# Optimization experiments

Hardware: AMD Instinct MI355X
Metric: run time of the kernel (lower is better)

## Reference

```python
import jax, jax.numpy as jnp
from jax import lax
import numpy as np

B, C, H, W = 8, 32, 512, 256
HEAD = 64
NUM_PEAKS, RADIUS, THRESH = 18, 5, 0.1
BN_EPS = 1e-5


def setup_inputs() -> dict:
    key = jax.random.key(0)
    ks = jax.random.split(key, 8)
    f32 = jnp.float32
    return {
        "x": jax.random.normal(ks[0], (B, C, H, W), f32),
        # fc_hm head params
        "w1_hm": jax.random.normal(ks[1], (HEAD, C, 3, 3), f32) * 0.05,
        "b1_hm": jnp.zeros((HEAD,), f32),
        "g_hm": jnp.ones((HEAD,), f32),
        "be_hm": jnp.zeros((HEAD,), f32),
        "m_hm": jnp.zeros((HEAD,), f32),
        "v_hm": jnp.ones((HEAD,), f32),
        "w2_hm": jax.random.normal(ks[2], (2, HEAD, 1, 1), f32) * 0.05,
        "b2_hm": jnp.zeros((2,), f32),
        # fc_vec head params
        "w1_vec": jax.random.normal(ks[3], (HEAD, C, 3, 3), f32) * 0.05,
        "b1_vec": jnp.zeros((HEAD,), f32),
        "g_vec": jnp.ones((HEAD,), f32),
        "be_vec": jnp.zeros((HEAD,), f32),
        "m_vec": jnp.zeros((HEAD,), f32),
        "v_vec": jnp.ones((HEAD,), f32),
        "w2_vec": jax.random.normal(ks[4], (2, HEAD, 1, 1), f32) * 0.05,
        "b2_vec": jnp.zeros((2,), f32),
    }


def _conv(x, w, b):
    y = lax.conv_general_dilated(x, w, (1, 1), 'SAME',
                                 dimension_numbers=('NCHW', 'OIHW', 'NCHW'))
    return y + b[None, :, None, None]


def _head(x, w1, b1, g, be, m, v, w2, b2):
    # conv3x3 -> BN(eval) -> ReLU -> (dropout=identity) -> conv final_kernel
    h = _conv(x, w1, b1)
    h = g[None, :, None, None] * (h - m[None, :, None, None]) \
        * lax.rsqrt(v + BN_EPS)[None, :, None, None] + be[None, :, None, None]
    h = jax.nn.relu(h)
    return _conv(h, w2, b2)


def _extract_peaks(hm):
    # hm: [H, W] -> peaks [NUM_PEAKS, 2] as (x, y); iterative argmax + square suppression
    ys = jnp.arange(H)[:, None]
    xs = jnp.arange(W)[None, :]

    def step(hmw, _):
        flat = hmw.reshape(-1)
        idx = jnp.argmax(flat)
        mval = flat[idx]
        y = idx // W
        x = idx % W
        valid = mval > THRESH
        peak = jnp.where(valid,
                         jnp.stack([x, y]).astype(hmw.dtype),
                         jnp.zeros((2,), hmw.dtype))
        sup = (jnp.abs(ys - y) <= RADIUS) & (jnp.abs(xs - x) <= RADIUS)
        hmw = jnp.where(valid & sup, jnp.zeros((), hmw.dtype), hmw)
        return hmw, peak

    _, peaks = lax.scan(step, hm, None, length=NUM_PEAKS)
    return peaks


def _order_points(points):
    # points: [N, 2]; pack valid points sorted by y descending, zeros at the end
    valid = points.sum(axis=1) != 0
    key_y = jnp.where(valid, points[:, 1], -jnp.inf)
    order = jnp.argsort(-key_y)
    p = points[order]
    return jnp.where(valid[order][:, None], p, jnp.zeros((), p.dtype))


def reference(x, w1_hm, b1_hm, g_hm, be_hm, m_hm, v_hm, w2_hm, b2_hm,
              w1_vec, b1_vec, g_vec, be_vec, m_vec, v_vec, w2_vec, b2_vec):
    dual_hm = jax.nn.sigmoid(_head(x, w1_hm, b1_hm, g_hm, be_hm, m_hm, v_hm, w2_hm, b2_hm))  # [B,2,H,W]
    vec_ind = _head(x, w1_vec, b1_vec, g_vec, be_vec, m_vec, v_vec, w2_vec, b2_vec)          # [B,2,H,W]

    peaks = jax.vmap(_extract_peaks)(dual_hm.reshape(B * 2, H, W)).reshape(B, 2, NUM_PEAKS, 2)
    upper = jax.vmap(_order_points)(peaks[:, 0])  # [B,18,2]
    lower = jax.vmap(_order_points)(peaks[:, 1])  # [B,18,2]
    mid = (upper + lower) / 2
    return dual_hm, upper, lower, mid, vec_ind
```

## Files before the change

### kernel.cpp

```cpp
#include <hip/hip_runtime.h>

typedef _Float16 f16;
typedef _Float16 f16x8 __attribute__((ext_vector_type(8)));
typedef float f32x4 __attribute__((ext_vector_type(4)));

#define Bn 8
#define Him 512
#define Wim 256
#define NPK 18
#define RAD 5
#define PTHRESH 0.1f
#define BN_EPS 1e-5f

#define SZ_HM   (Bn*2*Him*Wim)
#define OFF_UP  (SZ_HM)
#define OFF_LO  (OFF_UP + Bn*NPK*2)
#define OFF_MID (OFF_LO + Bn*NPK*2)
#define OFF_VEC (OFF_MID + Bn*NPK*2)

#define PH (Him + 2)
#define PW (Wim + 2)
#define XH_ELT ((size_t)Bn * PH * PW * 32)
#define XH_BYTES (XH_ELT * 2)
#define WBYTES 73728
#define WS_NEED (XH_BYTES + WBYTES + 4096)

#define WS_WBYTES 73728
#define XCOLS 258
#define XSTR  40

template <int CTRL>
__device__ __forceinline__ void red2_dpp(float& v, int& r) {
    int ov  = __builtin_amdgcn_update_dpp(0, __float_as_int(v), CTRL, 0xF, 0xF, true);
    int orr = __builtin_amdgcn_update_dpp(0, r, CTRL, 0xF, 0xF, true);
    float fv = __int_as_float(ov);
    if (fv > v || (fv == v && orr < r)) { v = fv; r = orr; }
}
__device__ __forceinline__ void red2_shfl(float& v, int& r, const int off) {
    float fv = __shfl_xor(v, off);
    int  orr = __shfl_xor(r, off);
    if (fv > v || (fv == v && orr < r)) { v = fv; r = orr; }
}
__device__ __forceinline__ void argred64(float& v, int& r) {
    red2_dpp<0xB1>(v, r);
    red2_dpp<0x4E>(v, r);
    red2_dpp<0x141>(v, r);
    red2_dpp<0x140>(v, r);
    red2_shfl(v, r, 16);
    red2_shfl(v, r, 32);
}


__global__ __launch_bounds__(256) void xform_kernel(
    const float* __restrict__ x, f16* __restrict__ xh)
{
    int e = blockIdx.x * 256 + threadIdx.x;
    if (e >= Bn * PH * PW * 4) return;
    int cb  = e & 3;
    int pxl = e >> 2;
    int b   = pxl / (PH * PW);
    int rem = pxl - b * (PH * PW);
    int yy  = rem / PW;
    int xx  = rem - yy * PW;
    int yv = yy - 1, xv = xx - 1;
    f16x8 hv;
    if ((unsigned)yv < (unsigned)Him && (unsigned)xv < (unsigned)Wim) {
        const float* sp = x + (((size_t)b * 32 + cb * 8) * Him + yv) * Wim + xv;
#pragma unroll
        for (int j = 0; j < 8; ++j) hv[j] = (f16)sp[(size_t)j * Him * Wim];
    } else {
#pragma unroll
        for (int j = 0; j < 8; ++j) hv[j] = (f16)0.f;
    }
    *(f16x8*)&xh[(size_t)pxl * 32 + cb * 8] = hv;
}

__global__ __launch_bounds__(256) void prep4_kernel(
    const float* __restrict__ w1_hm, const float* __restrict__ b1_hm,
    const float* __restrict__ g_hm,  const float* __restrict__ be_hm,
    const float* __restrict__ m_hm,  const float* __restrict__ v_hm,
    const float* __restrict__ w1_vec, const float* __restrict__ b1_vec,
    const float* __restrict__ g_vec,  const float* __restrict__ be_vec,
    const float* __restrict__ m_vec,  const float* __restrict__ v_vec,
    const float* __restrict__ w2_hm,  const float* __restrict__ w2_vec,
    void* __restrict__ wreg)
{
    f16* wf = (f16*)wreg;
    float* btf = (float*)((char*)wreg + WBYTES);
    float* waf = btf + 128;
    float* wbf = btf + 256;

    int e = blockIdx.x * 256 + threadIdx.x;
    int rs = e >> 12;
    int rem = e & 4095;
    int n = rem >> 5;
    int c = rem & 31;

    float g, vv, v;
    if (n < 64) { g = g_hm[n]; vv = v_hm[n]; v = w1_hm[(n * 32 + c) * 9 + rs]; }
    else { int j = n - 64; g = g_vec[j]; vv = v_vec[j]; v = w1_vec[(j * 32 + c) * 9 + rs]; }
    float al = g * rsqrtf(vv + BN_EPS);
    int byte = rs * 8192 + n * 64 + c * 2;
    byte ^= (n & 7) << 4;
    wf[byte >> 1] = (f16)(v * al);

    if (e < 128) {
        int nn = e;
        float gg, be, m, vvv, b1;
        if (nn < 64) { gg = g_hm[nn]; be = be_hm[nn]; m = m_hm[nn]; vvv = v_hm[nn]; b1 = b1_hm[nn]; }
        else { int j = nn - 64; gg = g_vec[j]; be = be_vec[j]; m = m_vec[j]; vvv = v_vec[j]; b1 = b1_vec[j]; }
        float a = gg * rsqrtf(vvv + BN_EPS);
        btf[nn] = a * (b1 - m) + be;
        if (nn < 64) { waf[nn] = w2_hm[nn]; wbf[nn] = w2_hm[64 + nn]; }
        else { int j = nn - 64; waf[nn] = w2_vec[j]; wbf[nn] = w2_vec[64 + j]; }
    }
}

__global__ __launch_bounds__(512, 2) void conv7_kernel(
    const f16* __restrict__ xh, const f16* __restrict__ wsw,
    const float* __restrict__ btf, const float* __restrict__ waf,
    const float* __restrict__ wbf,
    const float* __restrict__ b2_hm, const float* __restrict__ b2_vec,
    float* __restrict__ out)
{
    __shared__ __align__(16) f16 s_w[9 * 128 * 32];
    __shared__ __align__(16) f16 s_in[10 * 130 * 32];

    const int hw = blockIdx.x;
    const int logical = (hw & 7) * 128 + (hw >> 3);
    const int b    = logical >> 7;
    const int idx  = logical & 127;
    const int strip = idx >> 1;
    const int half  = idx & 1;
    const int y0  = strip * 8;
    const int x0h = half * 128;

    const int tid  = threadIdx.x;
    const int lane = tid & 63;
    const int wv   = tid >> 6;

    {
        const float4* src = (const float4*)wsw;
        float4* dst = (float4*)s_w;
#pragma unroll
        for (int i = 0; i < 9; ++i) dst[tid + 512 * i] = src[tid + 512 * i];
    }
    {
        const char* xb = (const char*)(xh + (size_t)b * PH * (PW * 32));
        char* sb = (char*)s_in;
        for (int i = tid; i < 5200; i += 512) {
            int row = i / 520;
            int r2  = i - row * 520;
            int px  = r2 >> 2;
            int bo  = (r2 & 3) << 4;
            f16x8 v = *(const f16x8*)(xb + (((size_t)(y0 + row) * PW + (x0h + px)) << 6) + bo);
            int la = ((row * 130 + px) << 6) + bo;
            la ^= (px & 7) << 4;
            *(f16x8*)(sb + la) = v;
        }
    }
    __syncthreads();

    const int l15 = lane & 15;
    const int g   = lane >> 4;
    const int khB = g << 4;
    const int sxz = ((l15 << 6) + khB) ^ ((l15 & 7) << 4);
    const char* swb = (const char*)s_w;
    const char* sib = (const char*)s_in;

    float* outhm  = out + ((size_t)b * 2) * Him * Wim + (y0 + wv) * Wim + x0h;
    float* outvec = out + OFF_VEC + ((size_t)b * 2) * Him * Wim + (y0 + wv) * Wim + x0h;

#pragma unroll 1
    for (int xseg = 0; xseg < 2; ++xseg) {
        const int px0s = xseg << 6;

        f32x4 acc[8][4];
#pragma unroll
        for (int ct = 0; ct < 8; ++ct)
#pragma unroll
            for (int nt = 0; nt < 4; ++nt) acc[ct][nt] = (f32x4){0.f, 0.f, 0.f, 0.f};

#pragma unroll 1
        for (int rr = 0; rr < 3; ++rr) {
#pragma unroll 1
            for (int ss = 0; ss < 3; ++ss) {
                f16x8 af[4];
#pragma unroll
                for (int nt = 0; nt < 4; ++nt) {
                    int pxl = px0s + nt * 16 + l15 + ss;
                    int la = (((wv + rr) * 130 + pxl) << 6) + khB;
                    la ^= (pxl & 7) << 4;
                    af[nt] = *(const f16x8*)(sib + la);
                }
                const char* wtap = swb + (rr * 3 + ss) * 8192 + sxz;
#pragma unroll
                for (int ct = 0; ct < 8; ++ct) {
                    f16x8 wfr = *(const f16x8*)(wtap + ct * 1024);
                    acc[ct][0] = __builtin_amdgcn_mfma_f32_16x16x32_f16(wfr, af[0], acc[ct][0], 0, 0, 0);
                    acc[ct][1] = __builtin_amdgcn_mfma_f32_16x16x32_f16(wfr, af[1], acc[ct][1], 0, 0, 0);
                    acc[ct][2] = __builtin_amdgcn_mfma_f32_16x16x32_f16(wfr, af[2], acc[ct][2], 0, 0, 0);
                    acc[ct][3] = __builtin_amdgcn_mfma_f32_16x16x32_f16(wfr, af[3], acc[ct][3], 0, 0, 0);
                }
            }
        }

        float s[4][4];
#pragma unroll
        for (int nt = 0; nt < 4; ++nt)
#pragma unroll
            for (int o = 0; o < 4; ++o) s[nt][o] = 0.f;

        const int cb0 = g << 2;
#pragma unroll
        for (int ct = 0; ct < 8; ++ct) {
            const float4 bt4 = *(const float4*)&btf[ct * 16 + cb0];
            const float4 wa4 = *(const float4*)&waf[ct * 16 + cb0];
            const float4 wb4 = *(const float4*)&wbf[ct * 16 + cb0];
            float btq[4] = { bt4.x, bt4.y, bt4.z, bt4.w };
            float waq[4] = { wa4.x, wa4.y, wa4.z, wa4.w };
            float wbq[4] = { wb4.x, wb4.y, wb4.z, wb4.w };
#pragma unroll
            for (int nt = 0; nt < 4; ++nt) {
#pragma unroll
                for (int q = 0; q < 4; ++q) {
                    float h = fmaxf(acc[ct][nt][q] + btq[q], 0.f);
                    if (ct < 4) {
                        s[nt][0] = fmaf(waq[q], h, s[nt][0]);
                        s[nt][1] = fmaf(wbq[q], h, s[nt][1]);
                    } else {
                        s[nt][2] = fmaf(waq[q], h, s[nt][2]);
                        s[nt][3] = fmaf(wbq[q], h, s[nt][3]);
                    }
                }
            }
        }
#pragma unroll
        for (int nt = 0; nt < 4; ++nt)
#pragma unroll
            for (int o = 0; o < 4; ++o) {
                s[nt][o] += __shfl_xor(s[nt][o], 16);
                s[nt][o] += __shfl_xor(s[nt][o], 32);
            }

        const float bh0 = b2_hm[0], bh1 = b2_hm[1], bv0 = b2_vec[0], bv1 = b2_vec[1];
        if (g == 0) {
#pragma unroll
            for (int nt = 0; nt < 4; ++nt) {
                int px = px0s + nt * 16 + l15;
                float e = __expf(-(s[nt][0] + bh0));
                outhm[px] = 1.f / (1.f + e);
            }
        } else if (g == 1) {
#pragma unroll
            for (int nt = 0; nt < 4; ++nt) {
                int px = px0s + nt * 16 + l15;
                float e = __expf(-(s[nt][1] + bh1));
                outhm[Him * Wim + px] = 1.f / (1.f + e);
            }
        } else if (g == 2) {
#pragma unroll
            for (int nt = 0; nt < 4; ++nt) {
                int px = px0s + nt * 16 + l15;
                outvec[px] = s[nt][2] + bv0;
            }
        } else {
#pragma unroll
            for (int nt = 0; nt < 4; ++nt) {
                int px = px0s + nt * 16 + l15;
                outvec[Him * Wim + px] = s[nt][3] + bv1;
            }
        }
    }
}

__global__ __launch_bounds__(1024) void peak_scan_kernel(
    const float* __restrict__ out, float* __restrict__ scanv, int* __restrict__ scanc)
{
    int m = blockIdx.x;
    const float* hm = out + (size_t)m * (Him * Wim);
    int tid  = threadIdx.x;
    int lane = tid & 63;
    int wv   = tid >> 6;
#pragma unroll 4
    for (int row = wv; row < 512; row += 16) {
        float4 v4 = *reinterpret_cast<const float4*>(hm + row * 256 + (lane << 2));
        float bv = v4.x; int bc = lane << 2;
        if (v4.y > bv) { bv = v4.y; bc = (lane << 2) + 1; }
        if (v4.z > bv) { bv = v4.z; bc = (lane << 2) + 2; }
        if (v4.w > bv) { bv = v4.w; bc = (lane << 2) + 3; }
        argred64(bv, bc);
        if (lane == 0) { scanv[(m << 9) + row] = bv; scanc[(m << 9) + row] = bc; }
    }
}

__global__ __launch_bounds__(64) void peak_iter_kernel(
    const float* __restrict__ scanv, const int* __restrict__ scanc,
    float* __restrict__ out)
{
    __shared__ float s_rv[512];
    __shared__ int   s_rc[512];
    __shared__ int   sbx[NPK], sby[NPK];
    __shared__ int   ppx[NPK], ppy[NPK];

    int m = blockIdx.x;
    int lane = threadIdx.x;
    const float* hm = out + (size_t)m * (Him * Wim);

#pragma unroll
    for (int k = 0; k < 8; ++k) {
        int r = lane + (k << 6);
        s_rv[r] = scanv[(m << 9) + r];
        s_rc[r] = scanc[(m << 9) + r];
    }
    if (lane < NPK) { ppx[lane] = 0; ppy[lane] = 0; }

    for (int it = 0; it < NPK; ++it) {
        float bv = s_rv[lane]; int br = lane;
#pragma unroll
        for (int k = 1; k < 8; ++k) {
            int r = lane + (k << 6);
            float v = s_rv[r];
            if (v > bv) { bv = v; br = r; }
        }
        argred64(bv, br);
        if (!(bv > PTHRESH)) break;

        int gy = br;
        int gc = s_rc[gy];
        if (lane == 0) { ppx[it] = gc; ppy[it] = gy; sbx[it] = gc; sby[it] = gy; }
        int nb = it + 1;

        float4 pre[11];
#pragma unroll
        for (int t = 0; t < 11; ++t) {
            int r = gy - RAD + t;
            if (r >= 0 && r < 512)
                pre[t] = *reinterpret_cast<const float4*>(hm + r * 256 + (lane << 2));
            else
                pre[t] = make_float4(0.f, 0.f, 0.f, 0.f);
        }

        bool needy = false;
        if (lane < 11) {
            int r0 = gy - RAD + lane;
            if (r0 >= 0 && r0 < 512) {
                int d = s_rc[r0] - gc; if (d < 0) d = -d;
                needy = (d <= RAD);
            }
        }
        unsigned long long mask = __ballot(needy);

#pragma unroll
        for (int t = 0; t < 11; ++t) {
            if (mask & (1ull << t)) {
                int r = gy - RAD + t;
                float vals[4] = { pre[t].x, pre[t].y, pre[t].z, pre[t].w };
                float bv2 = -1.f; int bc2 = 0;
#pragma unroll
                for (int q = 0; q < 4; ++q) {
                    int col = (lane << 2) + q;
                    float val = vals[q];
                    for (int i = 0; i < nb; ++i) {
                        int dy = r - sby[i]; if (dy < 0) dy = -dy;
                        int dx = col - sbx[i]; if (dx < 0) dx = -dx;
                        if (dy <= RAD && dx <= RAD) { val = 0.f; break; }
                    }
                    if (val > bv2) { bv2 = val; bc2 = col; }
                }
                argred64(bv2, bc2);
                if (lane == 0) { s_rv[r] = bv2; s_rc[r] = bc2; }
            }
        }
    }

    if (lane == 0) {
        float key[NPK]; int ord[NPK];
        for (int i = 0; i < NPK; ++i) {
            int valid = (ppx[i] + ppy[i]) != 0;
            key[i] = valid ? (float)ppy[i] : -3.4e38f;
            ord[i] = i;
        }
        for (int i = 1; i < NPK; ++i) {
            int oi = ord[i]; float ki = key[oi];
            int j = i - 1;
            while (j >= 0 && key[ord[j]] < ki) { ord[j + 1] = ord[j]; --j; }
            ord[j + 1] = oi;
        }
        int bb = m >> 1, which = m & 1;
        float* dst = out + (which ? OFF_LO : OFF_UP) + bb * (NPK * 2);
        for (int i = 0; i < NPK; ++i) {
            int src = ord[i];
            int valid = (ppx[src] + ppy[src]) != 0;
            dst[i * 2 + 0] = valid ? (float)ppx[src] : 0.f;
            dst[i * 2 + 1] = valid ? (float)ppy[src] : 0.f;
        }
    }
}


__global__ __launch_bounds__(256) void prep_fb_kernel(
    const float* __restrict__ w1_hm, const float* __restrict__ b1_hm,
    const float* __restrict__ g_hm,  const float* __restrict__ be_hm,
    const float* __restrict__ m_hm,  const float* __restrict__ v_hm,
    const float* __restrict__ w1_vec, const float* __restrict__ b1_vec,
    const float* __restrict__ g_vec,  const float* __restrict__ be_vec,
    const float* __restrict__ m_vec,  const float* __restrict__ v_vec,
    void* __restrict__ wsv)
{
    f16* wf = (f16*)wsv;
    float* alpha = (float*)((char*)wsv + WS_WBYTES);
    float* beta  = alpha + 128;
    int e = blockIdx.x * 256 + threadIdx.x;
    int rs = e >> 12;
    int rem = e & 4095;
    int n = rem >> 5;
    int c = rem & 31;
    float v;
    if (n < 64) v = w1_hm[(n * 32 + c) * 9 + rs];
    else        v = w1_vec[((n - 64) * 32 + c) * 9 + rs];
    wf[e] = (f16)v;
    if (e < 128) {
        int nn = e;
        float g, be, m, vv, b1;
        if (nn < 64) { g = g_hm[nn]; be = be_hm[nn]; m = m_hm[nn]; vv = v_hm[nn]; b1 = b1_hm[nn]; }
        else { int j = nn - 64; g = g_vec[j]; be = be_vec[j]; m = m_vec[j]; vv = v_vec[j]; b1 = b1_vec[j]; }
        float a = g * rsqrtf(vv + BN_EPS);
        alpha[nn] = a;
        beta[nn]  = a * (b1 - m) + be;
    }
}

__global__ __launch_bounds__(256, 1) void conv_fb_kernel(
    const float* __restrict__ x, const void* __restrict__ wsv,
    const float* __restrict__ w2_hm, const float* __restrict__ b2_hm,
    const float* __restrict__ w2_vec, const float* __restrict__ b2_vec,
    float* __restrict__ out)
{
    __shared__ __align__(16) f16 s_x[3 * XCOLS * XSTR];
    __shared__ __align__(16) f16 s_w[9 * 128 * 32];

    const int bid = blockIdx.x;
    const int y = bid & 511;
    const int b = bid >> 9;
    const int tid = threadIdx.x;
    const int lane = tid & 63;
    const int wv = tid >> 6;

    {
        const float4* src = (const float4*)wsv;
        float4* dst = (float4*)s_w;
#pragma unroll
        for (int i = 0; i < 18; ++i) dst[tid + 256 * i] = src[tid + 256 * i];
    }
    {
        const float* xb = x + (size_t)b * 32 * Him * Wim;
#pragma unroll 1
        for (int g = 0; g < 12; ++g) {
            int r  = g >> 2;
            int cb = (g & 3) << 3;
            int gy = y + r - 1;
            bool rowok = (gy >= 0) && (gy < Him);
            {
                int col = tid;
                int gx = col - 1;
                bool ok = rowok && (gx >= 0);
                f16x8 hv;
#pragma unroll
                for (int j = 0; j < 8; ++j) {
                    float v = ok ? xb[(size_t)(cb + j) * (Him * Wim) + gy * Wim + gx] : 0.f;
                    hv[j] = (f16)v;
                }
                *(f16x8*)&s_x[(r * XCOLS + col) * XSTR + cb] = hv;
            }
            if (tid < 2) {
                int col = 256 + tid;
                int gx = col - 1;
                bool ok = rowok && (gx < Wim);
                f16x8 hv;
#pragma unroll
                for (int j = 0; j < 8; ++j) {
                    float v = ok ? xb[(size_t)(cb + j) * (Him * Wim) + gy * Wim + gx] : 0.f;
                    hv[j] = (f16)v;
                }
                *(f16x8*)&s_x[(r * XCOLS + col) * XSTR + cb] = hv;
            }
        }
    }
    __syncthreads();

    const int px0 = wv * 64;
    const int l15 = lane & 15;
    const int khalf = (lane >> 4) << 3;

    f32x4 acc[4][8];
#pragma unroll
    for (int pt = 0; pt < 4; ++pt)
#pragma unroll
        for (int nt = 0; nt < 8; ++nt) acc[pt][nt] = (f32x4){0.f, 0.f, 0.f, 0.f};

#pragma unroll 1
    for (int rs = 0; rs < 9; ++rs) {
        const int rr = rs / 3, ss = rs % 3;
        f16x8 af[4];
#pragma unroll
        for (int pt = 0; pt < 4; ++pt) {
            int col = px0 + pt * 16 + l15 + ss;
            af[pt] = *(const f16x8*)&s_x[(rr * XCOLS + col) * XSTR + khalf];
        }
#pragma unroll
        for (int nt = 0; nt < 8; ++nt) {
            f16x8 bf = *(const f16x8*)&s_w[rs * 4096 + (nt * 16 + l15) * 32 + khalf];
            acc[0][nt] = __builtin_amdgcn_mfma_f32_16x16x32_f16(af[0], bf, acc[0][nt], 0, 0, 0);
            acc[1][nt] = __builtin_amdgcn_mfma_f32_16x16x32_f16(af[1], bf, acc[1][nt], 0, 0, 0);
            acc[2][nt] = __builtin_amdgcn_mfma_f32_16x16x32_f16(af[2], bf, acc[2][nt], 0, 0, 0);
            acc[3][nt] = __builtin_amdgcn_mfma_f32_16x16x32_f16(af[3], bf, acc[3][nt], 0, 0, 0);
        }
    }

    const float* alpha = (const float*)((const char*)wsv + WS_WBYTES);
    const float* beta  = alpha + 128;
    float al[8], bt[8], wa[8], wb[8];
#pragma unroll
    for (int nt = 0; nt < 8; ++nt) {
        int ch = nt * 16 + l15;
        al[nt] = alpha[ch];
        bt[nt] = beta[ch];
        int c6 = ch & 63;
        const float* w2 = (ch < 64) ? w2_hm : w2_vec;
        wa[nt] = w2[c6];
        wb[nt] = w2[64 + c6];
    }
    const float bh0 = b2_hm[0], bh1 = b2_hm[1], bv0 = b2_vec[0], bv1 = b2_vec[1];

    float* outhm  = out + ((size_t)b * 2) * Him * Wim + y * Wim;
    float* outvec = out + OFF_VEC + ((size_t)b * 2) * Him * Wim + y * Wim;

#pragma unroll
    for (int pt = 0; pt < 4; ++pt) {
#pragma unroll
        for (int q = 0; q < 4; ++q) {
            float s0 = 0.f, s1 = 0.f, s2 = 0.f, s3 = 0.f;
#pragma unroll
            for (int nt = 0; nt < 8; ++nt) {
                float h = fmaf(al[nt], acc[pt][nt][q], bt[nt]);
                h = fmaxf(h, 0.f);
                if (nt < 4) { s0 = fmaf(wa[nt], h, s0); s1 = fmaf(wb[nt], h, s1); }
                else        { s2 = fmaf(wa[nt], h, s2); s3 = fmaf(wb[nt], h, s3); }
            }
#pragma unroll
            for (int off = 1; off < 16; off <<= 1) {
                s0 += __shfl_xor(s0, off);
                s1 += __shfl_xor(s1, off);
                s2 += __shfl_xor(s2, off);
                s3 += __shfl_xor(s3, off);
            }
            int px = px0 + pt * 16 + ((lane >> 4) << 2) + q;
            if (l15 == 0) {
                outhm[px] = 1.f / (1.f + expf(-(s0 + bh0)));
            } else if (l15 == 1) {
                outhm[Him * Wim + px] = 1.f / (1.f + expf(-(s1 + bh1)));
            } else if (l15 == 2) {
                outvec[px] = s2 + bv0;
            } else if (l15 == 3) {
                outvec[Him * Wim + px] = s3 + bv1;
            }
        }
    }
}

__global__ __launch_bounds__(1024) void peak_fb_kernel(float* __restrict__ out)
{
    __shared__ float rowval[512];
    __shared__ int   rowcol[512];
    __shared__ int   sbx[NPK], sby[NPK];
    __shared__ int   ppx[NPK], ppy[NPK];

    int m = blockIdx.x;
    const float* hm = out + (size_t)m * (Him * Wim);
    int tid  = threadIdx.x;
    int lane = tid & 63;
    int wv   = tid >> 6;

    if (tid < NPK) { ppx[tid] = 0; ppy[tid] = 0; }

#pragma unroll 4
    for (int row = wv; row < 512; row += 16) {
        float4 v4 = *reinterpret_cast<const float4*>(hm + row * 256 + (lane << 2));
        float bv = v4.x; int bc = lane << 2;
        if (v4.y > bv) { bv = v4.y; bc = (lane << 2) + 1; }
        if (v4.z > bv) { bv = v4.z; bc = (lane << 2) + 2; }
        if (v4.w > bv) { bv = v4.w; bc = (lane << 2) + 3; }
        argred64(bv, bc);
        if (lane == 0) { rowval[row] = bv; rowcol[row] = bc; }
    }
    __syncthreads();

    if (wv != 0) return;

    for (int it = 0; it < NPK; ++it) {
        float bv = rowval[lane]; int br = lane;
#pragma unroll
        for (int k = 1; k < 8; ++k) {
            int r = lane + (k << 6);
            float v = rowval[r];
            if (v > bv) { bv = v; br = r; }
        }
        argred64(bv, br);
        if (!(bv > PTHRESH)) break;

        int gy = br;
        int gc = rowcol[gy];
        if (lane == 0) { ppx[it] = gc; ppy[it] = gy; sbx[it] = gc; sby[it] = gy; }
        int nb = it + 1;

        bool needy = false;
        if (lane < 11) {
            int r0 = gy - RAD + lane;
            if (r0 >= 0 && r0 < 512) {
                int d = rowcol[r0] - gc; if (d < 0) d = -d;
                needy = (d <= RAD);
            }
        }
        unsigned long long mask = __ballot(needy);

        while (mask) {
            int bit = __builtin_ctzll(mask);
            mask &= mask - 1;
            int r = gy - RAD + bit;
            float4 v4 = *reinterpret_cast<const float4*>(hm + r * 256 + (lane << 2));
            float vals[4] = { v4.x, v4.y, v4.z, v4.w };
            float bv2 = -1.f; int bc2 = 0;
#pragma unroll
            for (int q = 0; q < 4; ++q) {
                int col = (lane << 2) + q;
                float val = vals[q];
                for (int i = 0; i < nb; ++i) {
                    int dy = r - sby[i]; if (dy < 0) dy = -dy;
                    int dx = col - sbx[i]; if (dx < 0) dx = -dx;
                    if (dy <= RAD && dx <= RAD) { val = 0.f; break; }
                }
                if (val > bv2) { bv2 = val; bc2 = col; }
            }
            argred64(bv2, bc2);
            if (lane == 0) { rowval[r] = bv2; rowcol[r] = bc2; }
        }
    }

    if (tid == 0) {
        float key[NPK]; int ord[NPK];
        for (int i = 0; i < NPK; ++i) {
            int valid = (ppx[i] + ppy[i]) != 0;
            key[i] = valid ? (float)ppy[i] : -3.4e38f;
            ord[i] = i;
        }
        for (int i = 1; i < NPK; ++i) {
            int oi = ord[i]; float ki = key[oi];
            int j = i - 1;
            while (j >= 0 && key[ord[j]] < ki) { ord[j + 1] = ord[j]; --j; }
            ord[j + 1] = oi;
        }
        int bb = m >> 1, which = m & 1;
        float* dst = out + (which ? OFF_LO : OFF_UP) + bb * (NPK * 2);
        for (int i = 0; i < NPK; ++i) {
            int src = ord[i];
            int valid = (ppx[src] + ppy[src]) != 0;
            dst[i * 2 + 0] = valid ? (float)ppx[src] : 0.f;
            dst[i * 2 + 1] = valid ? (float)ppy[src] : 0.f;
        }
    }
}

__global__ __launch_bounds__(320) void mid_kernel(float* __restrict__ out)
{
    int t = threadIdx.x;
    if (t < Bn * NPK * 2)
        out[OFF_MID + t] = 0.5f * (out[OFF_UP + t] + out[OFF_LO + t]);
}

extern "C" void kernel_launch(void* const* d_in, const int* in_sizes, int n_in,
                              void* d_out, int out_size, void* d_ws, size_t ws_size,
                              hipStream_t stream)
{
    const float* x      = (const float*)d_in[0];
    const float* w1_hm  = (const float*)d_in[1];
    const float* b1_hm  = (const float*)d_in[2];
    const float* g_hm   = (const float*)d_in[3];
    const float* be_hm  = (const float*)d_in[4];
    const float* m_hm   = (const float*)d_in[5];
    const float* v_hm   = (const float*)d_in[6];
    const float* w2_hm  = (const float*)d_in[7];
    const float* b2_hm  = (const float*)d_in[8];
    const float* w1_vec = (const float*)d_in[9];
    const float* b1_vec = (const float*)d_in[10];
    const float* g_vec  = (const float*)d_in[11];
    const float* be_vec = (const float*)d_in[12];
    const float* m_vec  = (const float*)d_in[13];
    const float* v_vec  = (const float*)d_in[14];
    const float* w2_vec = (const float*)d_in[15];
    const float* b2_vec = (const float*)d_in[16];

    float* out = (float*)d_out;

    if (ws_size >= (size_t)WS_NEED) {
        f16*  xh   = (f16*)d_ws;
        char* wreg = (char*)d_ws + XH_BYTES;
        const float* btf = (const float*)(wreg + WBYTES);
        const float* waf = btf + 128;
        const float* wbf = btf + 256;

        xform_kernel<<<(Bn * PH * PW * 4 + 255) / 256, 256, 0, stream>>>(x, xh);
        prep4_kernel<<<144, 256, 0, stream>>>(
            w1_hm, b1_hm, g_hm, be_hm, m_hm, v_hm,
            w1_vec, b1_vec, g_vec, be_vec, m_vec, v_vec,
            w2_hm, w2_vec, wreg);
        conv7_kernel<<<1024, 512, 0, stream>>>(
            xh, (const f16*)wreg, btf, waf, wbf,
            b2_hm, b2_vec, out);

        float* scanv = (float*)d_ws;
        int*   scanc = (int*)((char*)d_ws + 32768);
        peak_scan_kernel<<<Bn * 2, 1024, 0, stream>>>(out, scanv, scanc);
        peak_iter_kernel<<<Bn * 2, 64, 0, stream>>>(scanv, scanc, out);
    } else {
        prep_fb_kernel<<<144, 256, 0, stream>>>(
            w1_hm, b1_hm, g_hm, be_hm, m_hm, v_hm,
            w1_vec, b1_vec, g_vec, be_vec, m_vec, v_vec, d_ws);
        conv_fb_kernel<<<Bn * Him, 256, 0, stream>>>(
            x, d_ws, w2_hm, b2_hm, w2_vec, b2_vec, out);
        peak_fb_kernel<<<Bn * 2, 1024, 0, stream>>>(out);
    }

    mid_kernel<<<1, 320, 0, stream>>>(out);
}
```

Before: 282.3 us.

## Replace row-scan peak search with histogram-threshold candidate pool greedy selection

Replaces the 16-block row-argmax scan plus single-wave iterative peak search with a pipeline: a per-map histogram of float bit patterns, a threshold chosen so at least 2080 candidates remain, compaction of those candidates into a packed key pool, and greedy max/suppress over the pool in shared memory. The aim is to spread the full-map read across 128 blocks and avoid rereading rows during the serial iterations. It adds four extra kernel launches and global atomics, and falls back to the old row-scan path when the pool would overflow.

```diff
diff --git a/kernel.cpp b/kernel.cpp
--- a/kernel.cpp
+++ b/kernel.cpp
@@ -3,6 +3,7 @@
 typedef _Float16 f16;
 typedef _Float16 f16x8 __attribute__((ext_vector_type(8)));
 typedef float f32x4 __attribute__((ext_vector_type(4)));
+typedef unsigned long long ull;
 
 #define Bn 8
 #define Him 512
@@ -10,6 +11,7 @@
 #define NPK 18
 #define RAD 5
 #define PTHRESH 0.1f
+#define TBITS 0x3DCCCCCDu
 #define BN_EPS 1e-5f
 
 #define SZ_HM   (Bn*2*Him*Wim)
@@ -24,6 +26,17 @@
 #define XH_BYTES (XH_ELT * 2)
 #define WBYTES 73728
 #define WS_NEED (XH_BYTES + WBYTES + 4096)
+
+#define NBIN 1024
+#define NCPY 8
+#define POOL_MIN 2080u
+#define POOL_CAP 6144
+#define WSU_HIST 0
+#define WSU_THR  16384
+#define WSU_CNT  16400
+#define WSU_FLAG 16416
+#define WSU_END  16432
+#define WSU_POOL 32768
 
 #define WS_WBYTES 73728
 #define XCOLS 258
@@ -48,6 +61,16 @@
     red2_dpp<0x140>(v, r);
     red2_shfl(v, r, 16);
     red2_shfl(v, r, 32);
+}
+__device__ __forceinline__ ull maxred64_u64(ull best) {
+#pragma unroll
+    for (int off = 32; off; off >>= 1) {
+        unsigned lo = (unsigned)best, hi = (unsigned)(best >> 32);
+        unsigned olo = __shfl_xor(lo, off), ohi = __shfl_xor(hi, off);
+        ull o = ((ull)ohi << 32) | olo;
+        if (o > best) best = o;
+    }
+    return best;
 }
 
 
@@ -274,88 +297,182 @@
     }
 }
 
-__global__ __launch_bounds__(1024) void peak_scan_kernel(
-    const float* __restrict__ out, float* __restrict__ scanv, int* __restrict__ scanc)
-{
-    int m = blockIdx.x;
-    const float* hm = out + (size_t)m * (Him * Wim);
-    int tid  = threadIdx.x;
-    int lane = tid & 63;
-    int wv   = tid >> 6;
-#pragma unroll 4
-    for (int row = wv; row < 512; row += 16) {
-        float4 v4 = *reinterpret_cast<const float4*>(hm + row * 256 + (lane << 2));
-        float bv = v4.x; int bc = lane << 2;
-        if (v4.y > bv) { bv = v4.y; bc = (lane << 2) + 1; }
-        if (v4.z > bv) { bv = v4.z; bc = (lane << 2) + 2; }
-        if (v4.w > bv) { bv = v4.w; bc = (lane << 2) + 3; }
-        argred64(bv, bc);
-        if (lane == 0) { scanv[(m << 9) + row] = bv; scanc[(m << 9) + row] = bc; }
-    }
-}
-
-__global__ __launch_bounds__(64) void peak_iter_kernel(
-    const float* __restrict__ scanv, const int* __restrict__ scanc,
-    float* __restrict__ out)
-{
-    __shared__ float s_rv[512];
-    __shared__ int   s_rc[512];
+
+__global__ __launch_bounds__(1024) void pzero_kernel(unsigned* __restrict__ ws)
+{
+    int t = threadIdx.x;
+    for (int i = t; i < WSU_END; i += 1024) ws[i] = 0u;
+}
+
+__global__ __launch_bounds__(1024) void phist_kernel(
+    const float* __restrict__ out, unsigned* __restrict__ ws)
+{
+    __shared__ unsigned h[NCPY][NBIN];
+    int t = threadIdx.x;
+    int m = blockIdx.x >> 3, sub = blockIdx.x & 7;
+    for (int i = t; i < NCPY * NBIN; i += 1024) ((unsigned*)h)[i] = 0u;
+    __syncthreads();
+    const float4* src = (const float4*)(out + (size_t)m * (Him * Wim) + sub * 16384);
+    unsigned* hc = h[(t >> 7) & 7];
+#pragma unroll
+    for (int p = 0; p < 4; ++p) {
+        float4 v = src[t + p * 1024];
+        atomicAdd(&hc[__float_as_uint(v.x) >> 21], 1u);
+        atomicAdd(&hc[__float_as_uint(v.y) >> 21], 1u);
+        atomicAdd(&hc[__float_as_uint(v.z) >> 21], 1u);
+        atomicAdd(&hc[__float_as_uint(v.w) >> 21], 1u);
+    }
+    __syncthreads();
+    unsigned s = 0;
+#pragma unroll
+    for (int c = 0; c < NCPY; ++c) s += h[c][t];
+    if (s) atomicAdd(&ws[WSU_HIST + m * NBIN + t], s);
+}
+
+__global__ __launch_bounds__(1024) void pthresh_kernel(unsigned* __restrict__ ws)
+{
+    __shared__ unsigned S[NBIN];
+    int t = threadIdx.x, m = blockIdx.x;
+    S[t] = ws[WSU_HIST + m * NBIN + t];
+    __syncthreads();
+    for (int off = 1; off < NBIN; off <<= 1) {
+        unsigned add = (t + off < NBIN) ? S[t + off] : 0u;
+        __syncthreads();
+        S[t] += add;
+        __syncthreads();
+    }
+    unsigned st  = S[t];
+    unsigned stn = (t + 1 < NBIN) ? S[t + 1] : 0u;
+    if (st >= POOL_MIN && (t == NBIN - 1 || stn < POOL_MIN)) {
+        ws[WSU_THR + m]  = (unsigned)t;
+        ws[WSU_FLAG + m] = (st > (unsigned)POOL_CAP) ? 1u : 0u;
+    }
+}
+
+__global__ __launch_bounds__(1024) void pcollect_kernel(
+    const float* __restrict__ out, unsigned* __restrict__ ws)
+{
+    int t = threadIdx.x;
+    int m = blockIdx.x >> 3, sub = blockIdx.x & 7;
+    unsigned thr = ws[WSU_THR + m];
+    ull* pool = (ull*)(ws + WSU_POOL) + (size_t)m * POOL_CAP;
+    unsigned* cnt = ws + WSU_CNT + m;
+    int base = sub * 16384;
+    const float4* src = (const float4*)(out + (size_t)m * (Him * Wim) + base);
+#pragma unroll
+    for (int p = 0; p < 4; ++p) {
+        int e4 = t + p * 1024;
+        float4 v = src[e4];
+        unsigned bx[4] = { __float_as_uint(v.x), __float_as_uint(v.y),
+                           __float_as_uint(v.z), __float_as_uint(v.w) };
+#pragma unroll
+        for (int q = 0; q < 4; ++q) {
+            if ((bx[q] >> 21) >= thr) {
+                unsigned pos = atomicAdd(cnt, 1u);
+                if (pos < (unsigned)POOL_CAP) {
+                    int idx = base + e4 * 4 + q;
+                    pool[pos] = ((ull)bx[q] << 17) | (ull)(131071 - idx);
+                }
+            }
+        }
+    }
+}
+
+__global__ __launch_bounds__(1024) void pgreedy_kernel(
+    const unsigned* __restrict__ ws, float* __restrict__ out)
+{
+    __shared__ ull  s_pool[POOL_CAP];
+    __shared__ float rowval[512];
+    __shared__ int   rowcol[512];
     __shared__ int   sbx[NPK], sby[NPK];
     __shared__ int   ppx[NPK], ppy[NPK];
 
     int m = blockIdx.x;
-    int lane = threadIdx.x;
+    int tid = threadIdx.x, lane = tid & 63, wv = tid >> 6;
     const float* hm = out + (size_t)m * (Him * Wim);
 
-#pragma unroll
-    for (int k = 0; k < 8; ++k) {
-        int r = lane + (k << 6);
-        s_rv[r] = scanv[(m << 9) + r];
-        s_rc[r] = scanc[(m << 9) + r];
-    }
-    if (lane < NPK) { ppx[lane] = 0; ppy[lane] = 0; }
-
-    for (int it = 0; it < NPK; ++it) {
-        float bv = s_rv[lane]; int br = lane;
-#pragma unroll
-        for (int k = 1; k < 8; ++k) {
-            int r = lane + (k << 6);
-            float v = s_rv[r];
-            if (v > bv) { bv = v; br = r; }
-        }
-        argred64(bv, br);
-        if (!(bv > PTHRESH)) break;
-
-        int gy = br;
-        int gc = s_rc[gy];
-        if (lane == 0) { ppx[it] = gc; ppy[it] = gy; sbx[it] = gc; sby[it] = gy; }
-        int nb = it + 1;
-
-        float4 pre[11];
-#pragma unroll
-        for (int t = 0; t < 11; ++t) {
-            int r = gy - RAD + t;
-            if (r >= 0 && r < 512)
-                pre[t] = *reinterpret_cast<const float4*>(hm + r * 256 + (lane << 2));
-            else
-                pre[t] = make_float4(0.f, 0.f, 0.f, 0.f);
-        }
-
-        bool needy = false;
-        if (lane < 11) {
-            int r0 = gy - RAD + lane;
-            if (r0 >= 0 && r0 < 512) {
-                int d = s_rc[r0] - gc; if (d < 0) d = -d;
-                needy = (d <= RAD);
-            }
-        }
-        unsigned long long mask = __ballot(needy);
-
-#pragma unroll
-        for (int t = 0; t < 11; ++t) {
-            if (mask & (1ull << t)) {
-                int r = gy - RAD + t;
-                float vals[4] = { pre[t].x, pre[t].y, pre[t].z, pre[t].w };
+    if (tid < NPK) { ppx[tid] = 0; ppy[tid] = 0; }
+
+    unsigned flag = ws[WSU_FLAG + m];
+
+    if (!flag) {
+        unsigned ncnt = ws[WSU_CNT + m];
+        int n = (ncnt < (unsigned)POOL_CAP) ? (int)ncnt : POOL_CAP;
+        int npad = (n + 63) & ~63;
+        const ull* pool = (const ull*)(ws + WSU_POOL) + (size_t)m * POOL_CAP;
+        for (int i = tid; i < npad; i += 1024) s_pool[i] = (i < n) ? pool[i] : 0ull;
+        __syncthreads();
+        if (wv != 0) return;
+
+        int nj = npad >> 6;
+        for (int it = 0; it < NPK; ++it) {
+            ull best = 0;
+            for (int j = 0; j < nj; ++j) {
+                ull k = s_pool[lane + (j << 6)];
+                if (k > best) best = k;
+            }
+            best = maxred64_u64(best);
+            if ((unsigned)(best >> 17) <= TBITS) break;
+            int idx = 131071 - (int)(best & 0x1FFFFull);
+            int py = idx >> 8, px = idx & 255;
+            if (lane == 0) { ppx[it] = px; ppy[it] = py; }
+            for (int j = 0; j < nj; ++j) {
+                int a = lane + (j << 6);
+                ull k = s_pool[a];
+                if (k) {
+                    int id2 = 131071 - (int)(k & 0x1FFFFull);
+                    int dy = (id2 >> 8) - py; dy = dy < 0 ? -dy : dy;
+                    int dx = (id2 & 255) - px; dx = dx < 0 ? -dx : dx;
+                    if (dy <= RAD && dx <= RAD) s_pool[a] = 0ull;
+                }
+            }
+        }
+    } else {
+#pragma unroll 4
+        for (int row = wv; row < 512; row += 16) {
+            float4 v4 = *reinterpret_cast<const float4*>(hm + row * 256 + (lane << 2));
+            float bv = v4.x; int bc = lane << 2;
+            if (v4.y > bv) { bv = v4.y; bc = (lane << 2) + 1; }
+            if (v4.z > bv) { bv = v4.z; bc = (lane << 2) + 2; }
+            if (v4.w > bv) { bv = v4.w; bc = (lane << 2) + 3; }
+            argred64(bv, bc);
+            if (lane == 0) { rowval[row] = bv; rowcol[row] = bc; }
+        }
+        __syncthreads();
+        if (wv != 0) return;
+
+        for (int it = 0; it < NPK; ++it) {
+            float bv = rowval[lane]; int br = lane;
+#pragma unroll
+            for (int k = 1; k < 8; ++k) {
+                int r = lane + (k << 6);
+                float v = rowval[r];
+                if (v > bv) { bv = v; br = r; }
+            }
+            argred64(bv, br);
+            if (!(bv > PTHRESH)) break;
+
+            int gy = br;
+            int gc = rowcol[gy];
+            if (lane == 0) { ppx[it] = gc; ppy[it] = gy; sbx[it] = gc; sby[it] = gy; }
+            int nb = it + 1;
+
+            bool needy = false;
+            if (lane < 11) {
+                int r0 = gy - RAD + lane;
+                if (r0 >= 0 && r0 < 512) {
+                    int d = rowcol[r0] - gc; if (d < 0) d = -d;
+                    needy = (d <= RAD);
+                }
+            }
+            unsigned long long mask = __ballot(needy);
+
+            while (mask) {
+                int bit = __builtin_ctzll(mask);
+                mask &= mask - 1;
+                int r = gy - RAD + bit;
+                float4 v4 = *reinterpret_cast<const float4*>(hm + r * 256 + (lane << 2));
+                float vals[4] = { v4.x, v4.y, v4.z, v4.w };
                 float bv2 = -1.f; int bc2 = 0;
 #pragma unroll
                 for (int q = 0; q < 4; ++q) {
@@ -369,12 +486,12 @@
                     if (val > bv2) { bv2 = val; bc2 = col; }
                 }
                 argred64(bv2, bc2);
-                if (lane == 0) { s_rv[r] = bv2; s_rc[r] = bc2; }
-            }
-        }
-    }
-
-    if (lane == 0) {
+                if (lane == 0) { rowval[r] = bv2; rowcol[r] = bc2; }
+            }
+        }
+    }
+
+    if (tid == 0) {
         float key[NPK]; int ord[NPK];
         for (int i = 0; i < NPK; ++i) {
             int valid = (ppx[i] + ppy[i]) != 0;
@@ -718,10 +835,12 @@
             xh, (const f16*)wreg, btf, waf, wbf,
             b2_hm, b2_vec, out);
 
-        float* scanv = (float*)d_ws;
-        int*   scanc = (int*)((char*)d_ws + 32768);
-        peak_scan_kernel<<<Bn * 2, 1024, 0, stream>>>(out, scanv, scanc);
-        peak_iter_kernel<<<Bn * 2, 64, 0, stream>>>(scanv, scanc, out);
+        unsigned* pws = (unsigned*)d_ws;
+        pzero_kernel<<<1, 1024, 0, stream>>>(pws);
+        phist_kernel<<<128, 1024, 0, stream>>>(out, pws);
+        pthresh_kernel<<<16, 1024, 0, stream>>>(pws);
+        pcollect_kernel<<<128, 1024, 0, stream>>>(out, pws);
+        pgreedy_kernel<<<16, 1024, 0, stream>>>(pws, out);
     } else {
         prep_fb_kernel<<<144, 256, 0, stream>>>(
             w1_hm, b1_hm, g_hm, be_hm, m_hm, v_hm,
```

Result: slower. 582.5 us (+106.3%).

## Defer row rescan to next iteration and keep row maxima in registers

Applied to the files above, without the earlier changes.

Row maxima move from shared memory into per-lane registers (v8). Affected rows are marked -1 right away, and their reloads are issued early so the rescan runs at the start of the next iteration, overlapping the global loads with the argmax. The argmax reduction now replaces its two final cross-half shuffles with four readlanes and a scalar compare. This is meant to cut shared memory traffic and hide load latency in a serial, latency-bound peak loop. The cost is more register pressure and subtler correctness: the deferred rows must be resolved before they can win the argmax, which holds because they are set to -1 before being rescanned.

```diff
diff --git a/kernel.cpp b/kernel.cpp
--- a/kernel.cpp
+++ b/kernel.cpp
@@ -3,6 +3,7 @@
 typedef _Float16 f16;
 typedef _Float16 f16x8 __attribute__((ext_vector_type(8)));
 typedef float f32x4 __attribute__((ext_vector_type(4)));
+typedef unsigned long long ull;
 
 #define Bn 8
 #define Him 512
@@ -48,6 +49,22 @@
     red2_dpp<0x140>(v, r);
     red2_shfl(v, r, 16);
     red2_shfl(v, r, 32);
+}
+__device__ __forceinline__ void argred64f(float& v, int& r) {
+    red2_dpp<0xB1>(v, r);
+    red2_dpp<0x4E>(v, r);
+    red2_dpp<0x141>(v, r);
+    red2_dpp<0x140>(v, r);
+    int vb = __float_as_int(v);
+    int b0 = __builtin_amdgcn_readlane(vb, 0),  q0 = __builtin_amdgcn_readlane(r, 0);
+    int b1 = __builtin_amdgcn_readlane(vb, 16), q1 = __builtin_amdgcn_readlane(r, 16);
+    int b2 = __builtin_amdgcn_readlane(vb, 32), q2 = __builtin_amdgcn_readlane(r, 32);
+    int b3 = __builtin_amdgcn_readlane(vb, 48), q3 = __builtin_amdgcn_readlane(r, 48);
+    int bb = b0, rr = q0;
+    if (b1 > bb || (b1 == bb && q1 < rr)) { bb = b1; rr = q1; }
+    if (b2 > bb || (b2 == bb && q2 < rr)) { bb = b2; rr = q2; }
+    if (b3 > bb || (b3 == bb && q3 < rr)) { bb = b3; rr = q3; }
+    v = __int_as_float(bb); r = rr;
 }
 
 
@@ -289,7 +306,7 @@
         if (v4.y > bv) { bv = v4.y; bc = (lane << 2) + 1; }
         if (v4.z > bv) { bv = v4.z; bc = (lane << 2) + 2; }
         if (v4.w > bv) { bv = v4.w; bc = (lane << 2) + 3; }
-        argred64(bv, bc);
+        argred64f(bv, bc);
         if (lane == 0) { scanv[(m << 9) + row] = bv; scanc[(m << 9) + row] = bc; }
     }
 }
@@ -298,48 +315,68 @@
     const float* __restrict__ scanv, const int* __restrict__ scanc,
     float* __restrict__ out)
 {
-    __shared__ float s_rv[512];
-    __shared__ int   s_rc[512];
-    __shared__ int   sbx[NPK], sby[NPK];
-    __shared__ int   ppx[NPK], ppy[NPK];
-
-    int m = blockIdx.x;
-    int lane = threadIdx.x;
+    __shared__ int s_rc[512];
+    __shared__ int sbx[NPK], sby[NPK];
+    __shared__ int ppx[NPK], ppy[NPK];
+
+    const int m = blockIdx.x;
+    const int lane = threadIdx.x;
     const float* hm = out + (size_t)m * (Him * Wim);
 
+    float v8[8];
 #pragma unroll
     for (int k = 0; k < 8; ++k) {
         int r = lane + (k << 6);
-        s_rv[r] = scanv[(m << 9) + r];
+        v8[k] = scanv[(m << 9) + r];
         s_rc[r] = scanc[(m << 9) + r];
     }
     if (lane < NPK) { ppx[lane] = 0; ppy[lane] = 0; }
 
+    unsigned pmask = 0;
+    int pgy = 0;
+    float4 pre[11];
+
     for (int it = 0; it < NPK; ++it) {
-        float bv = s_rv[lane]; int br = lane;
+        if (pmask) {
+            int nb = it;
+#pragma unroll
+            for (int t = 0; t < 11; ++t) {
+                if (pmask & (1u << t)) {
+                    int r = pgy - RAD + t;
+                    float vals[4] = { pre[t].x, pre[t].y, pre[t].z, pre[t].w };
+                    float bv2 = -1.f; int bc2 = 0;
+#pragma unroll
+                    for (int q = 0; q < 4; ++q) {
+                        int col = (lane << 2) + q;
+                        float val = vals[q];
+                        for (int i = 0; i < nb; ++i) {
+                            int dy = r - sby[i]; if (dy < 0) dy = -dy;
+                            int dx = col - sbx[i]; if (dx < 0) dx = -dx;
+                            if (dy <= RAD && dx <= RAD) { val = 0.f; break; }
+                        }
+                        if (val > bv2) { bv2 = val; bc2 = col; }
+                    }
+                    argred64f(bv2, bc2);
+                    if (lane == 0) s_rc[r] = bc2;
+                    if (lane == (r & 63)) v8[r >> 6] = bv2;
+                }
+            }
+            pmask = 0;
+        }
+
+        float bv = v8[0]; int br = lane;
 #pragma unroll
         for (int k = 1; k < 8; ++k) {
+            float v = v8[k];
             int r = lane + (k << 6);
-            float v = s_rv[r];
             if (v > bv) { bv = v; br = r; }
         }
-        argred64(bv, br);
+        argred64f(bv, br);
         if (!(bv > PTHRESH)) break;
 
         int gy = br;
         int gc = s_rc[gy];
         if (lane == 0) { ppx[it] = gc; ppy[it] = gy; sbx[it] = gc; sby[it] = gy; }
-        int nb = it + 1;
-
-        float4 pre[11];
-#pragma unroll
-        for (int t = 0; t < 11; ++t) {
-            int r = gy - RAD + t;
-            if (r >= 0 && r < 512)
-                pre[t] = *reinterpret_cast<const float4*>(hm + r * 256 + (lane << 2));
-            else
-                pre[t] = make_float4(0.f, 0.f, 0.f, 0.f);
-        }
 
         bool needy = false;
         if (lane < 11) {
@@ -349,27 +386,15 @@
                 needy = (d <= RAD);
             }
         }
-        unsigned long long mask = __ballot(needy);
-
+        ull bm = __ballot(needy);
+        pmask = (unsigned)bm & 0x7FFu;
+        pgy = gy;
 #pragma unroll
         for (int t = 0; t < 11; ++t) {
-            if (mask & (1ull << t)) {
+            if (pmask & (1u << t)) {
                 int r = gy - RAD + t;
-                float vals[4] = { pre[t].x, pre[t].y, pre[t].z, pre[t].w };
-                float bv2 = -1.f; int bc2 = 0;
-#pragma unroll
-                for (int q = 0; q < 4; ++q) {
-                    int col = (lane << 2) + q;
-                    float val = vals[q];
-                    for (int i = 0; i < nb; ++i) {
-                        int dy = r - sby[i]; if (dy < 0) dy = -dy;
-                        int dx = col - sbx[i]; if (dx < 0) dx = -dx;
-                        if (dy <= RAD && dx <= RAD) { val = 0.f; break; }
-                    }
-                    if (val > bv2) { bv2 = val; bc2 = col; }
-                }
-                argred64(bv2, bc2);
-                if (lane == 0) { s_rv[r] = bv2; s_rc[r] = bc2; }
+                pre[t] = *reinterpret_cast<const float4*>(hm + r * 256 + (lane << 2));
+                if (lane == (r & 63)) v8[r >> 6] = -1.f;
             }
         }
     }
```

Measured after the change: 273.1 us. -3.3%, faster.
